# Kernel optimization log

Hardware: AMD Instinct MI355X
Metric: run time of the kernel (lower is better)

Reference implementation:

```python
import jax, jax.numpy as jnp
import numpy as np

N, E, G = 50000, 400000, 64
IN_C, HID, OUT_C, HEADS = 256, 128, 256, 4
LRELU_SLOPE = 0.2
LN_EPS = 1e-5


def setup_inputs() -> dict:
    key = jax.random.key(0)
    ks = jax.random.split(key, 16)
    d = {}
    d["x"] = jax.random.normal(ks[0], (N, IN_C), dtype=jnp.float32)
    d["edge_index"] = jax.random.randint(ks[1], (2, E), 0, N, dtype=jnp.int32)
    d["batch"] = jnp.sort(jax.random.randint(ks[2], (N,), 0, G, dtype=jnp.int32))
    s1 = 1.0 / np.sqrt(IN_C)
    d["W1"] = jax.random.uniform(ks[3], (IN_C, HEADS * HID), jnp.float32, -s1, s1)
    d["att_src1"] = jax.random.normal(ks[4], (HEADS, HID), jnp.float32) * 0.1
    d["att_dst1"] = jax.random.normal(ks[5], (HEADS, HID), jnp.float32) * 0.1
    d["b1"] = jnp.zeros((HEADS * HID,), jnp.float32)
    d["ln1_g"] = jnp.ones((HEADS * HID,), jnp.float32)
    d["ln1_b"] = jnp.zeros((HEADS * HID,), jnp.float32)
    s2 = 1.0 / np.sqrt(HEADS * HID)
    d["W2"] = jax.random.uniform(ks[6], (HEADS * HID, OUT_C), jnp.float32, -s2, s2)
    d["att_src2"] = jax.random.normal(ks[7], (1, OUT_C), jnp.float32) * 0.1
    d["att_dst2"] = jax.random.normal(ks[8], (1, OUT_C), jnp.float32) * 0.1
    d["b2"] = jnp.zeros((OUT_C,), jnp.float32)
    d["ln2_g"] = jnp.ones((OUT_C,), jnp.float32)
    d["ln2_b"] = jnp.zeros((OUT_C,), jnp.float32)
    return d


def _layernorm(x, g, b):
    mu = jnp.mean(x, axis=-1, keepdims=True)
    var = jnp.mean(jnp.square(x - mu), axis=-1, keepdims=True)
    return (x - mu) * jax.lax.rsqrt(var + LN_EPS) * g + b


def _gat_conv(x, src, dst, W, a_src, a_dst, bias):
    # PyG GATConv (eval mode, dropout inactive), self-loops already in src/dst.
    H, C = a_src.shape
    h = (x @ W).reshape(N, H, C)                       # [N,H,C]
    e_src = jnp.einsum('nhc,hc->nh', h, a_src)          # [N,H]
    e_dst = jnp.einsum('nhc,hc->nh', h, a_dst)
    e = jax.nn.leaky_relu(e_src[src] + e_dst[dst], LRELU_SLOPE)  # [Etot,H]
    m = jax.ops.segment_max(e, dst, num_segments=N)     # segment softmax over incoming edges
    ex = jnp.exp(e - m[dst])
    s = jax.ops.segment_sum(ex, dst, num_segments=N)
    alpha = ex / (s[dst] + 1e-16)                       # [Etot,H]
    msg = h[src] * alpha[:, :, None]                    # [Etot,H,C]
    out = jax.ops.segment_sum(msg, dst, num_segments=N) # [N,H,C]
    return out.reshape(N, H * C) + bias


def reference(x, edge_index, batch, W1, att_src1, att_dst1, b1, ln1_g, ln1_b,
              W2, att_src2, att_dst2, b2, ln2_g, ln2_b):
    loops = jnp.arange(N, dtype=edge_index.dtype)
    src = jnp.concatenate([edge_index[0], loops])
    dst = jnp.concatenate([edge_index[1], loops])
    h = _gat_conv(x, src, dst, W1, att_src1, att_dst1, b1)
    h = _layernorm(h, ln1_g, ln1_b)
    h = jax.nn.relu(h)                                  # dropout is identity in eval
    h = _gat_conv(h, src, dst, W2, att_src2, att_dst2, b2)
    h = _layernorm(h, ln2_g, ln2_b)
    # global_mean_pool over graphs
    sums = jax.ops.segment_sum(h, batch, num_segments=G)
    cnts = jax.ops.segment_sum(jnp.ones((N,), h.dtype), batch, num_segments=G)
    return sums / jnp.maximum(cnts, 1.0)[:, None]
```

## Files before the change

### kernel.cpp

```cpp
#include <hip/hip_runtime.h>
#include <hip/hip_bf16.h>
#include <cstdint>

#define LRELU_SLOPE 0.2f

typedef short bf16x8 __attribute__((ext_vector_type(8)));
typedef float f32x4  __attribute__((ext_vector_type(4)));

__device__ __forceinline__ float b2f(unsigned short u) {
  return __uint_as_float(((unsigned int)u) << 16);
}
__device__ __forceinline__ unsigned short f2b(float f) {
  unsigned int u = __float_as_uint(f);
  return (unsigned short)((u + 0x7fff + ((u >> 16) & 1)) >> 16);
}

__device__ __forceinline__ void gload16(const void* g, void* l) {
  __builtin_amdgcn_global_load_lds(
      (const __attribute__((address_space(1))) unsigned int*)g,
      (__attribute__((address_space(3))) unsigned int*)l, 16, 0, 0);
}

__global__ __launch_bounds__(256)
void prep_x_count(const float* __restrict__ x, unsigned short* __restrict__ o,
                  int M, int Mpad, const int* __restrict__ ei, int E, int Etot,
                  int* __restrict__ count) {
  const int i = blockIdx.x * 256 + threadIdx.x;
  if (i < Mpad * 64) {
    const int row = i >> 6;
    const int c4  = (i & 63) * 4;
    ushort4 v = make_ushort4(0, 0, 0, 0);
    if (row < M) {
      const float4 f = *(const float4*)&x[(size_t)row * 256 + c4];
      v = make_ushort4(f2b(f.x), f2b(f.y), f2b(f.z), f2b(f.w));
    }
    *(ushort4*)&o[(size_t)row * 256 + c4] = v;
  }
  if (i < Etot) {
    const int d = (i < E) ? ei[E + i] : (i - E);
    atomicAdd(&count[d], 1);
  }
}

__global__ __launch_bounds__(256)
void cvt_wts(const float* __restrict__ W1, const float* __restrict__ W2,
             unsigned short* __restrict__ W1T, unsigned short* __restrict__ W2T) {
  int j = blockIdx.x * 256 + threadIdx.x;
  if (j < 512 * 256) {
    const int n = j >> 8, k = j & 255;
    W1T[j] = f2b(W1[(size_t)k * 512 + n]);
  } else {
    j -= 512 * 256;
    const int n = j >> 9, k = j & 511;
    W2T[j] = f2b(W2[(size_t)k * 256 + n]);
  }
}

__global__ __launch_bounds__(256)
void scan_blocksum(const int* __restrict__ count, int* __restrict__ bsum, int Nn) {
  const int i0 = blockIdx.x * 1024 + threadIdx.x * 4;
  int s = 0;
#pragma unroll
  for (int k = 0; k < 4; ++k) { const int i = i0 + k; if (i < Nn) s += count[i]; }
#pragma unroll
  for (int off = 1; off < 64; off <<= 1) s += __shfl_xor(s, off);
  __shared__ int ws[4];
  if ((threadIdx.x & 63) == 0) ws[threadIdx.x >> 6] = s;
  __syncthreads();
  if (threadIdx.x == 0) bsum[blockIdx.x] = ws[0] + ws[1] + ws[2] + ws[3];
}

__global__ __launch_bounds__(64)
void scan_top(const int* __restrict__ bsum, int* __restrict__ boff,
              int* __restrict__ rowptrN, int nb) {
  const int t = threadIdx.x;
  const int v = (t < nb) ? bsum[t] : 0;
  int incl = v;
#pragma unroll
  for (int off = 1; off < 64; off <<= 1) {
    const int u = __shfl_up(incl, off);
    if (t >= off) incl += u;
  }
  if (t < nb) boff[t] = incl - v;
  if (t == 63) *rowptrN = incl;
}

__global__ __launch_bounds__(256)
void scan_apply(const int* __restrict__ count, const int* __restrict__ boff,
                int* __restrict__ rowptr, int* __restrict__ cursor, int Nn) {
  const int t = threadIdx.x;
  const int lane = t & 63;
  const int w = t >> 6;
  const int i0 = blockIdx.x * 1024 + t * 4;
  int c[4]; int s = 0;
#pragma unroll
  for (int k = 0; k < 4; ++k) { const int i = i0 + k; c[k] = (i < Nn) ? count[i] : 0; s += c[k]; }
  int incl = s;
#pragma unroll
  for (int off = 1; off < 64; off <<= 1) {
    const int u = __shfl_up(incl, off);
    if (lane >= off) incl += u;
  }
  __shared__ int ws[4];
  if (lane == 63) ws[w] = incl;
  __syncthreads();
  int woff = 0;
  for (int k = 0; k < w; ++k) woff += ws[k];
  int base = boff[blockIdx.x] + woff + incl - s;
#pragma unroll
  for (int k = 0; k < 4; ++k) {
    const int i = i0 + k;
    if (i < Nn) { rowptr[i] = base; cursor[i] = base; base += c[k]; }
  }
}

__global__ __launch_bounds__(256)
void csr_scatter(const int* __restrict__ ei, int E, int Etot,
                 int* __restrict__ cursor, int* __restrict__ srcs,
                 int* __restrict__ dsts) {
  const int i = blockIdx.x * 256 + threadIdx.x;
  if (i >= Etot) return;
  const int s = (i < E) ? ei[i]     : (i - E);
  const int d = (i < E) ? ei[E + i] : (i - E);
  const int pos = atomicAdd(&cursor[d], 1);
  srcs[pos] = s;
  dsts[pos] = d;
}

template<int KSTEPS>
__global__ __launch_bounds__(256)
void gemm_bf16(const unsigned short* __restrict__ A,
               const unsigned short* __restrict__ BT,
               unsigned short* __restrict__ C, int M, int Nn, int K,
               const float* __restrict__ asrc, const float* __restrict__ adst,
               float* __restrict__ es, float* __restrict__ ed,
               int H, int lgC, int esPart) {
  __shared__ __align__(16) unsigned short smA[2][64 * 32];
  __shared__ __align__(16) unsigned short smB[2][128 * 32];
  const int tid  = threadIdx.x;
  const int lane = tid & 63;
  const int wid  = tid >> 6;
  const int wm = wid >> 1, wn = wid & 1;
  const int brow = blockIdx.y * 64;
  const int bcol = blockIdx.x * 128;
  const int u = lane >> 4, r15 = lane & 15;
  const int arow = tid >> 2, aslot = tid & 3;
  const size_t aBase = (size_t)(brow + arow) * K + (aslot ^ (arow & 3)) * 8;
  const int ldsA = arow * 32 + aslot * 8;
  const int brow0 = tid >> 2,        bslot0 = tid & 3;
  const int brow1 = (256 + tid) >> 2, bslot1 = tid & 3;
  const size_t bBase0 = (size_t)(bcol + brow0) * K + (bslot0 ^ (brow0 & 3)) * 8;
  const size_t bBase1 = (size_t)(bcol + brow1) * K + (bslot1 ^ (brow1 & 3)) * 8;
  const int ldsB0 = brow0 * 32 + bslot0 * 8;
  const int ldsB1 = brow1 * 32 + bslot1 * 8;

  auto stage = [&](int buf, int ks) {
    const int k0 = ks * 32;
    gload16(A + aBase + k0, &smA[buf][ldsA]);
    gload16(BT + bBase0 + k0, &smB[buf][ldsB0]);
    gload16(BT + bBase1 + k0, &smB[buf][ldsB1]);
  };

  f32x4 acc[2][4] = {};
  const int sw = u ^ (r15 & 3);

  stage(0, 0);
  asm volatile("s_waitcnt vmcnt(0)" ::: "memory");
  __syncthreads();
  int cur = 0;
#pragma unroll
  for (int ks = 0; ks < KSTEPS; ++ks) {
    if (ks + 1 < KSTEPS) stage(cur ^ 1, ks + 1);
    bf16x8 af[2], bfv[4];
#pragma unroll
    for (int m = 0; m < 2; ++m) {
      const int row = wm * 32 + m * 16 + r15;
      af[m] = *(const bf16x8*)&smA[cur][row * 32 + sw * 8];
    }
#pragma unroll
    for (int n = 0; n < 4; ++n) {
      const int col = wn * 64 + n * 16 + r15;
      bfv[n] = *(const bf16x8*)&smB[cur][col * 32 + sw * 8];
    }
#pragma unroll
    for (int m = 0; m < 2; ++m)
#pragma unroll
      for (int n = 0; n < 4; ++n)
        acc[m][n] = __builtin_amdgcn_mfma_f32_16x16x32_bf16(
            af[m], bfv[n], acc[m][n], 0, 0, 0);
    if (ks + 1 < KSTEPS) {
      asm volatile("s_waitcnt vmcnt(0)" ::: "memory");
      __syncthreads();
      cur ^= 1;
    }
  }

  __syncthreads();
  unsigned short* cb = &smB[0][0];
#pragma unroll
  for (int m = 0; m < 2; ++m)
#pragma unroll
    for (int n = 0; n < 4; ++n) {
      const int col = wn * 64 + n * 16 + r15;
#pragma unroll
      for (int rr = 0; rr < 4; ++rr) {
        const int row = wm * 32 + m * 16 + u * 4 + rr;
        cb[row * 128 + col] = f2b(acc[m][n][rr]);
      }
    }
  __syncthreads();
#pragma unroll
  for (int i = 0; i < 4; ++i) {
    const int idx = (i * 256 + tid) * 8;
    const int row = idx >> 7;
    const int cc  = idx & 127;
    const int grow = brow + row;
    if (grow < M)
      *(float4*)&C[(size_t)grow * Nn + bcol + cc] = *(const float4*)&cb[idx];
  }

  es += (size_t)blockIdx.x * esPart;
  ed += (size_t)blockIdx.x * esPart;
  const int head = bcol >> lgC;
  float asv[4], adv[4];
#pragma unroll
  for (int n = 0; n < 4; ++n) {
    const int cc = bcol + wn * 64 + n * 16 + r15;
    asv[n] = asrc[cc];
    adv[n] = adst[cc];
  }
#pragma unroll
  for (int m = 0; m < 2; ++m) {
#pragma unroll
    for (int rr = 0; rr < 4; ++rr) {
      float pes = 0.f, ped = 0.f;
#pragma unroll
      for (int n = 0; n < 4; ++n) {
        pes = fmaf(acc[m][n][rr], asv[n], pes);
        ped = fmaf(acc[m][n][rr], adv[n], ped);
      }
#pragma unroll
      for (int off = 1; off < 16; off <<= 1) {
        pes += __shfl_xor(pes, off);
        ped += __shfl_xor(ped, off);
      }
      if (r15 == 0) {
        const int row = brow + wm * 32 + m * 16 + u * 4 + rr;
        if (row < M) {
          unsafeAtomicAdd(&es[row * H + head], pes);
          unsafeAtomicAdd(&ed[row * H + head], ped);
        }
      }
    }
  }
}

template<int H>
__global__ __launch_bounds__(256)
void ex_compute(const int* __restrict__ srcs, const int* __restrict__ dsts,
                const float* __restrict__ es, const float* __restrict__ ed,
                float* __restrict__ exCSR, int Etot, int pN) {
  const int p = blockIdx.x * 256 + threadIdx.x;
  if (p >= Etot) return;
  const int sN = srcs[p], dN = dsts[p];
  if constexpr (H == 4) {
    const float4 a = *(const float4*)&es[sN * 4];
    const float4 b = *(const float4*)&ed[dN * 4];
    float e0 = a.x + b.x, e1 = a.y + b.y, e2 = a.z + b.z, e3 = a.w + b.w;
    e0 = (e0 > 0.f) ? e0 : LRELU_SLOPE * e0;
    e1 = (e1 > 0.f) ? e1 : LRELU_SLOPE * e1;
    e2 = (e2 > 0.f) ? e2 : LRELU_SLOPE * e2;
    e3 = (e3 > 0.f) ? e3 : LRELU_SLOPE * e3;
    *(float4*)&exCSR[p * 4] =
        make_float4(__expf(e0), __expf(e1), __expf(e2), __expf(e3));
  } else {
    float e = (es[sN] + es[pN + sN]) + (ed[dN] + ed[pN + dN]);
    e = (e > 0.f) ? e : LRELU_SLOPE * e;
    exCSR[p] = __expf(e);
  }
}

template<int H, int C, bool RELU, bool BFOUT>
__global__ __launch_bounds__(256)
void gat_agg_ln(const int* __restrict__ rowptr, const int* __restrict__ srcs,
                const float* __restrict__ exCSR,
                const unsigned short* __restrict__ h,
                const float* __restrict__ bias, const float* __restrict__ lng,
                const float* __restrict__ lnb, unsigned short* __restrict__ obf,
                float* __restrict__ of32, int Nn) {
  constexpr int HC = H * C;
  constexpr int F  = HC / 64;
  const int wave = threadIdx.x >> 6;
  const int lane = threadIdx.x & 63;
  const int n = blockIdx.x * 4 + wave;
  if (n >= Nn) return;
  const int beg = rowptr[n];
  const int deg = rowptr[n + 1] - beg;
  const int hl = (lane * F) / C;

  float dsum = 0.f;
  if constexpr (H == 4) {
    for (int it = lane; it < deg * 4; it += 64) dsum += exCSR[beg * 4 + it];
#pragma unroll
    for (int off = 4; off < 64; off <<= 1) dsum += __shfl_xor(dsum, off);
    dsum = __shfl(dsum, hl);
  } else {
    for (int it = lane; it < deg; it += 64) dsum += exCSR[beg + it];
#pragma unroll
    for (int off = 1; off < 64; off <<= 1) dsum += __shfl_xor(dsum, off);
  }
  const float inv_s = 1.0f / (dsum + 1e-16f);

  float acc[F];
#pragma unroll
  for (int i = 0; i < F; ++i) acc[i] = 0.f;

  auto fma_rows = [&](const ushort4* v0, const ushort4* v1, const float* a, int cnt) {
    for (int q = 0; q < cnt; ++q) {
      acc[0] = fmaf(b2f(v0[q].x), a[q], acc[0]);
      acc[1] = fmaf(b2f(v0[q].y), a[q], acc[1]);
      acc[2] = fmaf(b2f(v0[q].z), a[q], acc[2]);
      acc[3] = fmaf(b2f(v0[q].w), a[q], acc[3]);
      if constexpr (F == 8) {
        acc[4] = fmaf(b2f(v1[q].x), a[q], acc[4]);
        acc[5] = fmaf(b2f(v1[q].y), a[q], acc[5]);
        acc[6] = fmaf(b2f(v1[q].z), a[q], acc[6]);
        acc[7] = fmaf(b2f(v1[q].w), a[q], acc[7]);
      }
    }
  };

  int j = 0;
  for (; j + 4 <= deg; j += 4) {
    int s4[4];
    float a4[4];
#pragma unroll
    for (int q = 0; q < 4; ++q) s4[q] = srcs[beg + j + q];
#pragma unroll
    for (int q = 0; q < 4; ++q) a4[q] = exCSR[(beg + j + q) * H + hl] * inv_s;
    ushort4 v0[4], v1[4];
#pragma unroll
    for (int q = 0; q < 4; ++q) {
      const unsigned short* hp = &h[(size_t)s4[q] * HC + lane * F];
      v0[q] = *(const ushort4*)hp;
      if constexpr (F == 8) v1[q] = *(const ushort4*)(hp + 4);
    }
    fma_rows(v0, v1, a4, 4);
  }
  for (; j < deg; ++j) {
    const int src = srcs[beg + j];
    const float a = exCSR[(beg + j) * H + hl] * inv_s;
    const unsigned short* hp = &h[(size_t)src * HC + lane * F];
    ushort4 v0 = *(const ushort4*)hp, v1;
    if constexpr (F == 8) v1 = *(const ushort4*)(hp + 4);
    fma_rows(&v0, &v1, &a, 1);
  }

#pragma unroll
  for (int i = 0; i < F; i += 4) {
    const float4 bb = *(const float4*)&bias[lane * F + i];
    acc[i + 0] += bb.x; acc[i + 1] += bb.y;
    acc[i + 2] += bb.z; acc[i + 3] += bb.w;
  }
  float sum = 0.f, sq = 0.f;
#pragma unroll
  for (int i = 0; i < F; ++i) { sum += acc[i]; sq += acc[i] * acc[i]; }
#pragma unroll
  for (int off = 1; off < 64; off <<= 1) {
    sum += __shfl_xor(sum, off);
    sq  += __shfl_xor(sq, off);
  }
  const float mu  = sum / HC;
  const float var = sq / HC - mu * mu;
  const float r   = rsqrtf(var + 1e-5f);
  float y[F];
#pragma unroll
  for (int i = 0; i < F; i += 4) {
    const float4 gg = *(const float4*)&lng[lane * F + i];
    const float4 bl = *(const float4*)&lnb[lane * F + i];
    y[i + 0] = (acc[i + 0] - mu) * r * gg.x + bl.x;
    y[i + 1] = (acc[i + 1] - mu) * r * gg.y + bl.y;
    y[i + 2] = (acc[i + 2] - mu) * r * gg.z + bl.z;
    y[i + 3] = (acc[i + 3] - mu) * r * gg.w + bl.w;
  }
  if constexpr (RELU) {
#pragma unroll
    for (int i = 0; i < F; ++i) y[i] = fmaxf(y[i], 0.f);
  }
  if constexpr (BFOUT) {
    unsigned short* op = &obf[(size_t)n * HC + lane * F];
    *(ushort4*)op = make_ushort4(f2b(y[0]), f2b(y[1]), f2b(y[2]), f2b(y[3]));
    if constexpr (F == 8)
      *(ushort4*)(op + 4) = make_ushort4(f2b(y[4]), f2b(y[5]), f2b(y[6]), f2b(y[7]));
  } else {
    float* op = &of32[(size_t)n * HC + lane * F];
    *(float4*)op = make_float4(y[0], y[1], y[2], y[3]);
    if constexpr (F == 8)
      *(float4*)(op + 4) = make_float4(y[4], y[5], y[6], y[7]);
  }
}

__global__ __launch_bounds__(256)
void pool_partial(const unsigned short* __restrict__ x, const int* __restrict__ batch,
                  float* __restrict__ tmp, int* __restrict__ cnt, int Nn) {
  const int r0 = blockIdx.x * 64;
  const int rend = min(r0 + 64, Nn);
  const int t = threadIdx.x;
  float acc = 0.f;
  int cur = batch[r0];
  int seglen = 0;
  for (int r = r0; r < rend; ++r) {
    const int g = batch[r];
    if (g != cur) {
      unsafeAtomicAdd(&tmp[cur * 256 + t], acc);
      if (t == 0) atomicAdd(&cnt[cur], seglen);
      acc = 0.f; seglen = 0; cur = g;
    }
    acc += b2f(x[(size_t)r * 256 + t]);
    ++seglen;
  }
  unsafeAtomicAdd(&tmp[cur * 256 + t], acc);
  if (t == 0) atomicAdd(&cnt[cur], seglen);
}

__global__ __launch_bounds__(256)
void pool_final(const float* __restrict__ tmp, const int* __restrict__ cnt,
                float* __restrict__ out) {
  const int g = blockIdx.x;
  const int t = threadIdx.x;
  out[g * 256 + t] = tmp[g * 256 + t] / fmaxf((float)cnt[g], 1.f);
}

extern "C" void kernel_launch(void* const* d_in, const int* in_sizes, int n_in,
                              void* d_out, int out_size, void* d_ws, size_t ws_size,
                              hipStream_t stream) {
  const float* x    = (const float*)d_in[0];
  const int*   ei   = (const int*)d_in[1];
  const int*   batch= (const int*)d_in[2];
  const float* W1   = (const float*)d_in[3];
  const float* as1  = (const float*)d_in[4];
  const float* ad1  = (const float*)d_in[5];
  const float* b1   = (const float*)d_in[6];
  const float* g1   = (const float*)d_in[7];
  const float* be1  = (const float*)d_in[8];
  const float* W2   = (const float*)d_in[9];
  const float* as2  = (const float*)d_in[10];
  const float* ad2  = (const float*)d_in[11];
  const float* b2   = (const float*)d_in[12];
  const float* g2   = (const float*)d_in[13];
  const float* be2  = (const float*)d_in[14];

  const int N    = in_sizes[0] / 256;
  const int E    = in_sizes[1] / 2;
  const int Etot = E + N;
  const int Mpad = ((N + 63) / 64) * 64;
  const int NB   = (N + 1023) / 1024;

  float* ws = (float*)d_ws;
  unsigned short* out2 = (unsigned short*)ws;
  unsigned short* A2bf = out2 + (size_t)N * 256;
  unsigned short* A1bf = A2bf;
  unsigned short* h1bf = A2bf + (size_t)Mpad * 512;
  unsigned short* W1T  = h1bf + (size_t)N * 512;
  unsigned short* W2T  = W1T + 512 * 256;
  float* es1 = (float*)(W2T + 512 * 256);
  float* ed1 = es1 + (size_t)N * 4;
  float* es2 = ed1 + (size_t)N * 4;
  float* ed2 = es2 + (size_t)N * 2;
  int* count  = (int*)(ed2 + (size_t)N * 2);
  int* rowptr = count + N;
  int* cursor = rowptr + N + 4;
  int* srcs   = cursor + N;
  int* dsts   = srcs + Etot;
  float* exCSR = (float*)(dsts + Etot);
  float* ptmp = exCSR + (size_t)Etot * 4;
  int*   pcnt = (int*)(ptmp + 64 * 256);
  int*   bsum = pcnt + 64;
  int*   boff = bsum + 64;
  unsigned short* h2bf = h1bf;

  const int eb = (Etot + 255) / 256;

  hipMemsetAsync(es1, 0, (size_t)N * 13 * 4, stream);
  hipMemsetAsync(ptmp, 0, (size_t)(64 * 256 + 64) * 4, stream);
  hipMemsetAsync(A2bf + (size_t)N * 512, 0, (size_t)(Mpad - N) * 512 * 2, stream);

  prep_x_count<<<(Mpad * 64 + 255) / 256, 256, 0, stream>>>(
      x, A1bf, N, Mpad, ei, E, Etot, count);
  cvt_wts<<<(2 * 512 * 256 + 255) / 256, 256, 0, stream>>>(W1, W2, W1T, W2T);

  scan_blocksum<<<NB, 256, 0, stream>>>(count, bsum, N);
  scan_top<<<1, 64, 0, stream>>>(bsum, boff, &rowptr[N], NB);
  scan_apply<<<NB, 256, 0, stream>>>(count, boff, rowptr, cursor, N);
  csr_scatter<<<eb, 256, 0, stream>>>(ei, E, Etot, cursor, srcs, dsts);

  gemm_bf16<8><<<dim3(4, Mpad / 64), 256, 0, stream>>>(
      A1bf, W1T, h1bf, N, 512, 256, as1, ad1, es1, ed1, 4, 7, 0);
  ex_compute<4><<<eb, 256, 0, stream>>>(srcs, dsts, es1, ed1, exCSR, Etot, 0);
  gat_agg_ln<4, 128, true, true><<<(N + 3) / 4, 256, 0, stream>>>(
      rowptr, srcs, exCSR, h1bf, b1, g1, be1, A2bf, nullptr, N);

  gemm_bf16<16><<<dim3(2, Mpad / 64), 256, 0, stream>>>(
      A2bf, W2T, h2bf, N, 256, 512, as2, ad2, es2, ed2, 1, 8, N);
  ex_compute<1><<<eb, 256, 0, stream>>>(srcs, dsts, es2, ed2, exCSR, Etot, N);
  gat_agg_ln<1, 256, false, true><<<(N + 3) / 4, 256, 0, stream>>>(
      rowptr, srcs, exCSR, h2bf, b2, g2, be2, out2, nullptr, N);

  pool_partial<<<(N + 63) / 64, 256, 0, stream>>>(out2, batch, ptmp, pcnt, N);
  pool_final<<<64, 256, 0, stream>>>(ptmp, pcnt, (float*)d_out);
}
```

Before: 319.2 us.

## Remap GEMM blocks per XCD, widen gather loads, use nontemporal stores

The GEMM grid becomes 1D, and block IDs are remapped so the column tiles of a row tile land on the same XCD. The aim is to share A-tile reuse in that XCD's L2. The GEMM output and the aggregation output now use nontemporal stores. The aggregation gather unrolls to 8 edges with single 16-byte or 8-byte loads per row and unpacks bf16 pairs with shifts and masks. The changes trade more register pressure and padding blocks that exit early for better locality and more memory-level parallelism.

```diff
diff --git a/kernel.cpp b/kernel.cpp
--- a/kernel.cpp
+++ b/kernel.cpp
@@ -6,6 +6,8 @@
 
 typedef short bf16x8 __attribute__((ext_vector_type(8)));
 typedef float f32x4  __attribute__((ext_vector_type(4)));
+typedef unsigned int u32x4 __attribute__((ext_vector_type(4)));
+typedef unsigned int u32x2 __attribute__((ext_vector_type(2)));
 
 __device__ __forceinline__ float b2f(unsigned short u) {
   return __uint_as_float(((unsigned int)u) << 16);
@@ -13,6 +15,9 @@
 __device__ __forceinline__ unsigned short f2b(float f) {
   unsigned int u = __float_as_uint(f);
   return (unsigned short)((u + 0x7fff + ((u >> 16) & 1)) >> 16);
+}
+__device__ __forceinline__ unsigned int pk2(float a, float b) {
+  return (unsigned int)f2b(a) | ((unsigned int)f2b(b) << 16);
 }
 
 __device__ __forceinline__ void gload16(const void* g, void* l) {
@@ -127,27 +132,34 @@
   dsts[pos] = d;
 }
 
-template<int KSTEPS>
+template<int KSTEPS, int NBCOL>
 __global__ __launch_bounds__(256)
 void gemm_bf16(const unsigned short* __restrict__ A,
                const unsigned short* __restrict__ BT,
                unsigned short* __restrict__ C, int M, int Nn, int K,
                const float* __restrict__ asrc, const float* __restrict__ adst,
                float* __restrict__ es, float* __restrict__ ed,
-               int H, int lgC, int esPart) {
+               int H, int lgC, int esPart, int nbRow) {
+  const int bid = blockIdx.x;
+  const int xcd = bid & 7;
+  const int j   = bid >> 3;
+  const int browT = xcd + 8 * (j / NBCOL);
+  const int bcolT = j % NBCOL;
+  if (browT >= nbRow) return;
+  const int brow = browT * 64;
+  const int bcol = bcolT * 128;
+
   __shared__ __align__(16) unsigned short smA[2][64 * 32];
   __shared__ __align__(16) unsigned short smB[2][128 * 32];
   const int tid  = threadIdx.x;
   const int lane = tid & 63;
   const int wid  = tid >> 6;
   const int wm = wid >> 1, wn = wid & 1;
-  const int brow = blockIdx.y * 64;
-  const int bcol = blockIdx.x * 128;
   const int u = lane >> 4, r15 = lane & 15;
   const int arow = tid >> 2, aslot = tid & 3;
   const size_t aBase = (size_t)(brow + arow) * K + (aslot ^ (arow & 3)) * 8;
   const int ldsA = arow * 32 + aslot * 8;
-  const int brow0 = tid >> 2,        bslot0 = tid & 3;
+  const int brow0 = tid >> 2,         bslot0 = tid & 3;
   const int brow1 = (256 + tid) >> 2, bslot1 = tid & 3;
   const size_t bBase0 = (size_t)(bcol + brow0) * K + (bslot0 ^ (brow0 & 3)) * 8;
   const size_t bBase1 = (size_t)(bcol + brow1) * K + (bslot1 ^ (brow1 & 3)) * 8;
@@ -216,11 +228,12 @@
     const int cc  = idx & 127;
     const int grow = brow + row;
     if (grow < M)
-      *(float4*)&C[(size_t)grow * Nn + bcol + cc] = *(const float4*)&cb[idx];
-  }
-
-  es += (size_t)blockIdx.x * esPart;
-  ed += (size_t)blockIdx.x * esPart;
+      __builtin_nontemporal_store(*(const u32x4*)&cb[idx],
+                                  (u32x4*)&C[(size_t)grow * Nn + bcol + cc]);
+  }
+
+  es += (size_t)bcolT * esPart;
+  ed += (size_t)bcolT * esPart;
   const int head = bcol >> lgC;
   float asv[4], adv[4];
 #pragma unroll
@@ -315,45 +328,57 @@
 #pragma unroll
   for (int i = 0; i < F; ++i) acc[i] = 0.f;
 
-  auto fma_rows = [&](const ushort4* v0, const ushort4* v1, const float* a, int cnt) {
-    for (int q = 0; q < cnt; ++q) {
-      acc[0] = fmaf(b2f(v0[q].x), a[q], acc[0]);
-      acc[1] = fmaf(b2f(v0[q].y), a[q], acc[1]);
-      acc[2] = fmaf(b2f(v0[q].z), a[q], acc[2]);
-      acc[3] = fmaf(b2f(v0[q].w), a[q], acc[3]);
-      if constexpr (F == 8) {
-        acc[4] = fmaf(b2f(v1[q].x), a[q], acc[4]);
-        acc[5] = fmaf(b2f(v1[q].y), a[q], acc[5]);
-        acc[6] = fmaf(b2f(v1[q].z), a[q], acc[6]);
-        acc[7] = fmaf(b2f(v1[q].w), a[q], acc[7]);
+  auto fma_pack = [&](unsigned int w, float a, int i) {
+    acc[i]     = fmaf(__uint_as_float(w << 16), a, acc[i]);
+    acc[i + 1] = fmaf(__uint_as_float(w & 0xffff0000u), a, acc[i + 1]);
+  };
+
+  int j = 0;
+  for (; j + 8 <= deg; j += 8) {
+    int s8[8];
+#pragma unroll
+    for (int q = 0; q < 8; ++q) s8[q] = srcs[beg + j + q];
+    if constexpr (F == 8) {
+      uint4 g[8];
+#pragma unroll
+      for (int q = 0; q < 8; ++q)
+        g[q] = *(const uint4*)&h[(size_t)s8[q] * HC + lane * 8];
+      float a8[8];
+#pragma unroll
+      for (int q = 0; q < 8; ++q) a8[q] = exCSR[(beg + j + q) * H + hl] * inv_s;
+#pragma unroll
+      for (int q = 0; q < 8; ++q) {
+        fma_pack(g[q].x, a8[q], 0);
+        fma_pack(g[q].y, a8[q], 2);
+        fma_pack(g[q].z, a8[q], 4);
+        fma_pack(g[q].w, a8[q], 6);
       }
-    }
-  };
-
-  int j = 0;
-  for (; j + 4 <= deg; j += 4) {
-    int s4[4];
-    float a4[4];
-#pragma unroll
-    for (int q = 0; q < 4; ++q) s4[q] = srcs[beg + j + q];
-#pragma unroll
-    for (int q = 0; q < 4; ++q) a4[q] = exCSR[(beg + j + q) * H + hl] * inv_s;
-    ushort4 v0[4], v1[4];
-#pragma unroll
-    for (int q = 0; q < 4; ++q) {
-      const unsigned short* hp = &h[(size_t)s4[q] * HC + lane * F];
-      v0[q] = *(const ushort4*)hp;
-      if constexpr (F == 8) v1[q] = *(const ushort4*)(hp + 4);
-    }
-    fma_rows(v0, v1, a4, 4);
+    } else {
+      uint2 g[8];
+#pragma unroll
+      for (int q = 0; q < 8; ++q)
+        g[q] = *(const uint2*)&h[(size_t)s8[q] * HC + lane * 4];
+      float a8[8];
+#pragma unroll
+      for (int q = 0; q < 8; ++q) a8[q] = exCSR[(beg + j + q) * H + hl] * inv_s;
+#pragma unroll
+      for (int q = 0; q < 8; ++q) {
+        fma_pack(g[q].x, a8[q], 0);
+        fma_pack(g[q].y, a8[q], 2);
+      }
+    }
   }
   for (; j < deg; ++j) {
     const int src = srcs[beg + j];
     const float a = exCSR[(beg + j) * H + hl] * inv_s;
-    const unsigned short* hp = &h[(size_t)src * HC + lane * F];
-    ushort4 v0 = *(const ushort4*)hp, v1;
-    if constexpr (F == 8) v1 = *(const ushort4*)(hp + 4);
-    fma_rows(&v0, &v1, &a, 1);
+    if constexpr (F == 8) {
+      const uint4 g = *(const uint4*)&h[(size_t)src * HC + lane * 8];
+      fma_pack(g.x, a, 0); fma_pack(g.y, a, 2);
+      fma_pack(g.z, a, 4); fma_pack(g.w, a, 6);
+    } else {
+      const uint2 g = *(const uint2*)&h[(size_t)src * HC + lane * 4];
+      fma_pack(g.x, a, 0); fma_pack(g.y, a, 2);
+    }
   }
 
 #pragma unroll
@@ -389,9 +414,14 @@
   }
   if constexpr (BFOUT) {
     unsigned short* op = &obf[(size_t)n * HC + lane * F];
-    *(ushort4*)op = make_ushort4(f2b(y[0]), f2b(y[1]), f2b(y[2]), f2b(y[3]));
-    if constexpr (F == 8)
-      *(ushort4*)(op + 4) = make_ushort4(f2b(y[4]), f2b(y[5]), f2b(y[6]), f2b(y[7]));
+    if constexpr (F == 8) {
+      u32x4 v = {pk2(y[0], y[1]), pk2(y[2], y[3]),
+                 pk2(y[4], y[5]), pk2(y[6], y[7])};
+      __builtin_nontemporal_store(v, (u32x4*)op);
+    } else {
+      u32x2 v = {pk2(y[0], y[1]), pk2(y[2], y[3])};
+      __builtin_nontemporal_store(v, (u32x2*)op);
+    }
   } else {
     float* op = &of32[(size_t)n * HC + lane * F];
     *(float4*)op = make_float4(y[0], y[1], y[2], y[3]);
@@ -454,6 +484,8 @@
   const int E    = in_sizes[1] / 2;
   const int Etot = E + N;
   const int Mpad = ((N + 63) / 64) * 64;
+  const int nb   = Mpad / 64;
+  const int nbp  = ((nb + 7) / 8) * 8;
   const int NB   = (N + 1023) / 1024;
 
   float* ws = (float*)d_ws;
@@ -494,14 +526,14 @@
   scan_apply<<<NB, 256, 0, stream>>>(count, boff, rowptr, cursor, N);
   csr_scatter<<<eb, 256, 0, stream>>>(ei, E, Etot, cursor, srcs, dsts);
 
-  gemm_bf16<8><<<dim3(4, Mpad / 64), 256, 0, stream>>>(
-      A1bf, W1T, h1bf, N, 512, 256, as1, ad1, es1, ed1, 4, 7, 0);
+  gemm_bf16<8, 4><<<nbp * 4, 256, 0, stream>>>(
+      A1bf, W1T, h1bf, N, 512, 256, as1, ad1, es1, ed1, 4, 7, 0, nb);
   ex_compute<4><<<eb, 256, 0, stream>>>(srcs, dsts, es1, ed1, exCSR, Etot, 0);
   gat_agg_ln<4, 128, true, true><<<(N + 3) / 4, 256, 0, stream>>>(
       rowptr, srcs, exCSR, h1bf, b1, g1, be1, A2bf, nullptr, N);
 
-  gemm_bf16<16><<<dim3(2, Mpad / 64), 256, 0, stream>>>(
-      A2bf, W2T, h2bf, N, 256, 512, as2, ad2, es2, ed2, 1, 8, N);
+  gemm_bf16<16, 2><<<nbp * 2, 256, 0, stream>>>(
+      A2bf, W2T, h2bf, N, 256, 512, as2, ad2, es2, ed2, 1, 8, N, nb);
   ex_compute<1><<<eb, 256, 0, stream>>>(srcs, dsts, es2, ed2, exCSR, Etot, N);
   gat_agg_ln<1, 256, false, true><<<(N + 3) / 4, 256, 0, stream>>>(
       rowptr, srcs, exCSR, h2bf, b2, g2, be2, out2, nullptr, N);
```

Result: slower. 365.8 us (+14.6%).
